# Performance work log

Hardware: AMD Instinct MI355X
Metric: run time of the kernel (lower is better)

The kernel has to match this reference:

```python
import jax, jax.numpy as jnp
import numpy as np

B, T, D = 2, 2048, 2048
H, HKV, DH = 16, 4, 128  # n_heads, n_kv_heads, d_head
EPS = 1e-6


def _rms_norm(t):
    # normalize over last dim, no learned weight (matches F.rms_norm default)
    return t * jax.lax.rsqrt(jnp.mean(t * t, axis=-1, keepdims=True) + EPS)


def _ortho_rope(t, cos, sin):
    # t: (b, h, t, d); unfold(-1,2,2) -> even/odd pairs
    x0 = t[..., 0::2]  # (b,h,t,d/2)
    x1 = t[..., 1::2]
    y0 = x0 * cos - x1 * sin
    y1 = x1 * cos + x0 * sin
    # NOTE: concatenated halves (NOT re-interleaved), faithful to source
    return jnp.concatenate((y0, y1), axis=-1)


def setup_inputs() -> dict:
    key = jax.random.key(0)
    ks = jax.random.split(key, 10)
    return {
        "x": jax.random.normal(ks[0], (B, T, D), jnp.float32),
        "pos_ids": jnp.broadcast_to(jnp.arange(T, dtype=jnp.int64), (B, T)),
        "cos": jax.random.normal(ks[1], (T, DH // 2), jnp.float32),
        "sin": jax.random.normal(ks[2], (T, DH // 2), jnp.float32),
        "v1": jax.random.normal(ks[3], (B, HKV, T, DH), jnp.float32),
        "Wq": jax.random.normal(ks[4], (H * DH, D), jnp.float32) * (D ** -0.5),
        "Wk": jax.random.normal(ks[5], (HKV * DH, D), jnp.float32) * (D ** -0.5),
        "Wv": jax.random.normal(ks[6], (HKV * DH, D), jnp.float32) * (D ** -0.5),
        "Wo": jax.random.normal(ks[7], (D, D), jnp.float32) * (D ** -0.5),
        "gate_w": jax.random.normal(ks[8], (H, H), jnp.float32) * 0.1,
        "v_lamb": jnp.float32(0.5),
    }


def reference(x, pos_ids, cos, sin, v1, Wq, Wk, Wv, Wo, gate_w, v_lamb):
    b, t, _ = x.shape
    # fused QKV projections (Linear, no bias: x @ W.T), split to heads
    q = (x @ Wq.T).reshape(b, t, H, DH).transpose(0, 2, 1, 3)    # (b,H,t,d)
    k = (x @ Wk.T).reshape(b, t, HKV, DH).transpose(0, 2, 1, 3)  # (b,Hkv,t,d)
    v = (x @ Wv.T).reshape(b, t, HKV, DH).transpose(0, 2, 1, 3)
    # value residual: lerp(v, v1, lamb) = v + lamb*(v1 - v)
    v = v + v_lamb * (v1 - v)
    # QK RMSNorm then ortho RoPE
    q = _ortho_rope(_rms_norm(q), cos, sin)
    k = _ortho_rope(_rms_norm(k), cos, sin)
    # kv_cache.upsert modeled as prefill: k,v unchanged, causal block mask
    g = H // HKV  # GQA group size
    k = jnp.repeat(k, g, axis=1)  # (b,H,t,d)
    vfull = jnp.repeat(v, g, axis=1)
    scale = DH ** -0.5
    scores = jnp.einsum('bhqd,bhkd->bhqk', q, k) * scale
    causal = jnp.tril(jnp.ones((t, t), dtype=bool))
    scores = jnp.where(causal, scores, jnp.finfo(scores.dtype).min)
    attn = jax.nn.softmax(scores, axis=-1)
    y = jnp.einsum('bhqk,bhkd->bhqd', attn, vfull)  # (b,H,t,d)
    # per-head sigmoid gate from first n_heads channels of x
    gates = jax.nn.sigmoid(x[..., :H] @ gate_w.T)   # (b,t,H)
    y = y * gates.transpose(0, 2, 1)[..., None]     # (b,H,t,1)
    y = y.transpose(0, 2, 1, 3).reshape(b, t, H * DH)
    out = y @ Wo.T
    return (out, v1)
```

## Files before the change

### kernel.cpp

```cpp
#include <hip/hip_runtime.h>

typedef __bf16 bf16;
typedef __attribute__((ext_vector_type(8))) __bf16 bf16x8;
typedef __attribute__((ext_vector_type(4))) __bf16 bf16x4;
typedef __attribute__((ext_vector_type(4))) float f32x4;
typedef __attribute__((ext_vector_type(4))) short short4v;
typedef __attribute__((ext_vector_type(4))) unsigned int u32x4;

#define BB 2
#define TT 2048
#define DD 2048
#define HH 16
#define HKV 4
#define DHD 128
#define NQKV 3072

__device__ __forceinline__ void gl_lds16(const bf16* g, bf16* l) {
    __builtin_amdgcn_global_load_lds(
        (const __attribute__((address_space(1))) void*)g,
        (__attribute__((address_space(3))) void*)l, 16, 0, 0);
}

__global__ void cvt_bf16(const float* __restrict__ src, bf16* __restrict__ dst, int n8) {
    int i = blockIdx.x * 256 + threadIdx.x;
    if (i >= n8) return;
    float4 a = ((const float4*)src)[i * 2];
    float4 b = ((const float4*)src)[i * 2 + 1];
    bf16x8 v;
    v[0] = (bf16)a.x; v[1] = (bf16)a.y; v[2] = (bf16)a.z; v[3] = (bf16)a.w;
    v[4] = (bf16)b.x; v[5] = (bf16)b.y; v[6] = (bf16)b.z; v[7] = (bf16)b.w;
    *(bf16x8*)(dst + (size_t)i * 8) = v;
}

template <int MODE>
__global__ void gemm_bt(const bf16* __restrict__ A, const bf16* __restrict__ Bw,
                        int M, int N, int K,
                        float* __restrict__ Cout,
                        bf16* __restrict__ qb, bf16* __restrict__ kb,
                        bf16* __restrict__ vtb,
                        const float* __restrict__ v1,
                        const float* __restrict__ cosb,
                        const float* __restrict__ sinb,
                        const float* __restrict__ lamp) {
    constexpr int SMEM_ELE = (MODE == 1) ? 17920 : 16384;
    __shared__ bf16 smem[SMEM_ELE];
    bf16* As = smem;
    bf16* Bs = smem + 8192;
    const int tid = threadIdx.x;
    const int w = tid >> 6, lane = tid & 63;
    const int l15 = lane & 15, quad = lane >> 4;
    const int m0 = blockIdx.y * 128, n0 = blockIdx.x * 128;
    const int wm = (w & 1) * 64, wn = (w >> 1) * 64;

    f32x4 acc[4][4] = {};
    const int lrow = lane >> 2;
    const int lcol = (lane & 3) * 8;

    for (int k0 = 0; k0 < K; k0 += 64) {
#pragma unroll
        for (int i = 0; i < 4; i++) {
            int c = w * 4 + i;
            int kc2 = c >> 3, rc = c & 7;
            int row = rc * 16 + lrow;
            int kk = k0 + kc2 * 32 + lcol;
            gl_lds16(A + (size_t)(m0 + row) * K + kk, As + c * 512);
            gl_lds16(Bw + (size_t)(n0 + row) * K + kk, Bs + c * 512);
        }
        __syncthreads();
#pragma unroll
        for (int kc2 = 0; kc2 < 2; kc2++) {
            bf16x8 af[4], bfr[4];
#pragma unroll
            for (int mi = 0; mi < 4; mi++)
                af[mi] = *(const bf16x8*)(As + kc2 * 4096 + ((wm >> 4) + mi) * 512 + l15 * 32 + quad * 8);
#pragma unroll
            for (int ni = 0; ni < 4; ni++)
                bfr[ni] = *(const bf16x8*)(Bs + kc2 * 4096 + ((wn >> 4) + ni) * 512 + l15 * 32 + quad * 8);
#pragma unroll
            for (int mi = 0; mi < 4; mi++)
#pragma unroll
                for (int ni = 0; ni < 4; ni++)
                    acc[mi][ni] = __builtin_amdgcn_mfma_f32_16x16x32_bf16(af[mi], bfr[ni], acc[mi][ni], 0, 0, 0);
        }
        __syncthreads();
    }

    if constexpr (MODE == 0) {
#pragma unroll
        for (int mi = 0; mi < 4; mi++)
#pragma unroll
            for (int ni = 0; ni < 4; ni++)
#pragma unroll
                for (int r = 0; r < 4; r++) {
                    int m = m0 + wm + mi * 16 + quad * 4 + r;
                    int n = n0 + wn + ni * 16 + l15;
                    Cout[(size_t)m * N + n] = acc[mi][ni][r];
                }
    } else {
        const int hid = n0 >> 7;
        const int b = m0 >> 11;
        const int t0 = m0 & (TT - 1);
        bf16* ep = smem;

        if (hid < 20) {
            float* ssum = (float*)(smem + 17408);
            float ssq[4][4];
#pragma unroll
            for (int mi = 0; mi < 4; mi++)
#pragma unroll
                for (int r = 0; r < 4; r++) {
                    float s = 0.f;
#pragma unroll
                    for (int ni = 0; ni < 4; ni++) {
                        float v = acc[mi][ni][r];
                        s += v * v;
                    }
                    s += __shfl_xor(s, 1);
                    s += __shfl_xor(s, 2);
                    s += __shfl_xor(s, 4);
                    s += __shfl_xor(s, 8);
                    ssq[mi][r] = s;
                }
            if (l15 == 0) {
#pragma unroll
                for (int mi = 0; mi < 4; mi++)
#pragma unroll
                    for (int r = 0; r < 4; r++)
                        ssum[(wn >> 6) * 128 + wm + mi * 16 + quad * 4 + r] = ssq[mi][r];
            }
            __syncthreads();
            const float QSCALE = 0.08838834764831845f * 1.4426950408889634f;
            float rn[4][4];
#pragma unroll
            for (int mi = 0; mi < 4; mi++)
#pragma unroll
                for (int r = 0; r < 4; r++) {
                    int row = wm + mi * 16 + quad * 4 + r;
                    float ss = ssum[row] + ssum[128 + row];
                    float rv = rsqrtf(ss * (1.f / 128.f) + 1e-6f);
                    if (hid < HH) rv *= QSCALE;
                    rn[mi][r] = rv;
                }
#pragma unroll
            for (int mi = 0; mi < 4; mi++)
#pragma unroll
                for (int ni = 0; ni < 4; ni++)
#pragma unroll
                    for (int r = 0; r < 4; r++) {
                        float sv = acc[mi][ni][r] * rn[mi][r];
                        float pv = __shfl_xor(sv, 1);
                        int nl = wn + ni * 16 + l15;
                        int j = nl >> 1;
                        int tl = wm + mi * 16 + quad * 4 + r;
                        float c = cosb[(size_t)(t0 + tl) * 64 + j];
                        float s = sinb[(size_t)(t0 + tl) * 64 + j];
                        float o = (nl & 1) ? (sv * c + pv * s) : (sv * c - pv * s);
                        int oc = (nl & 1) ? (64 + j) : j;
                        ep[tl * 136 + oc] = (bf16)o;
                    }
            __syncthreads();
            bf16* dst = (hid < HH)
                ? (qb + ((size_t)(b * HH + hid) * TT + t0) * DHD)
                : (kb + ((size_t)(b * HKV + (hid - HH)) * TT + t0) * DHD);
            int tl = tid >> 1, half = tid & 1;
#pragma unroll
            for (int c8 = 0; c8 < 8; c8++)
                *(bf16x8*)(dst + (size_t)tl * DHD + half * 64 + c8 * 8) =
                    *(const bf16x8*)(ep + tl * 136 + half * 64 + c8 * 8);
        } else {
            float lam = lamp[0];
            int vh = hid - 20;
            const float* v1b = v1 + ((size_t)(b * HKV + vh) * TT) * DHD;
#pragma unroll
            for (int mi = 0; mi < 4; mi++)
#pragma unroll
                for (int ni = 0; ni < 4; ni++)
#pragma unroll
                    for (int r = 0; r < 4; r++) {
                        int d = wn + ni * 16 + l15;
                        int tl = wm + mi * 16 + quad * 4 + r;
                        float val = acc[mi][ni][r];
                        float vm = val + lam * (v1b[(size_t)(t0 + tl) * DHD + d] - val);
                        ep[d * 136 + tl] = (bf16)vm;
                    }
            __syncthreads();
            bf16* dstv = vtb + ((size_t)(b * HKV + vh) * DHD) * TT + t0;
            int dd = tid >> 1, half = tid & 1;
#pragma unroll
            for (int c8 = 0; c8 < 8; c8++)
                *(bf16x8*)(dstv + (size_t)dd * TT + half * 64 + c8 * 8) =
                    *(const bf16x8*)(ep + dd * 136 + half * 64 + c8 * 8);
        }
    }
}

__global__ void gatesk(const float* __restrict__ x, const float* __restrict__ gw,
                       float* __restrict__ gates) {
    __shared__ float gws[256];
    gws[threadIdx.x] = gw[threadIdx.x];
    __syncthreads();
    int idx = blockIdx.x * 256 + threadIdx.x;
    int h = idx & 15, token = idx >> 4;
    const float* xr = x + (size_t)token * DD;
    float z = 0.f;
#pragma unroll
    for (int j = 0; j < 16; j++) z += xr[j] * gws[h * 16 + j];
    gates[idx] = 1.f / (1.f + __expf(-z));
}

__global__ __launch_bounds__(512, 2) void fattn(const bf16* __restrict__ qbuf,
                                                const bf16* __restrict__ kbuf,
                                                const bf16* __restrict__ vt,
                                                const float* __restrict__ gates,
                                                bf16* __restrict__ yb) {
    __shared__ bf16 Ks[2][4 * 2048];
    __shared__ bf16 VTs[2][8192];

    const int bid = blockIdx.x;
    const int bh = bid & 31;
    const int g = bid >> 5;
    const int h = bh & 15, b = bh >> 4;
    const int hk = h >> 2;
    const int tid = threadIdx.x, w = tid >> 6, lane = tid & 63;
    const int wq = w & 3, grp = w >> 2;
    const int l15 = lane & 15, quad = lane >> 4;

    const bf16* qbase = qbuf + ((size_t)(b * HH + h) * TT) * DHD;
    const bf16* kbase = kbuf + ((size_t)(b * HKV + hk) * TT) * DHD;
    const bf16* vtbase = vt + ((size_t)(b * HKV + hk) * DHD) * TT;

    const int Tq0 = grp ? (15 - g) : g;
    const int Tq1 = grp ? (16 + g) : (31 - g);
    const int ktmax_blk = 31 - g;

    bf16x8 qf0[4], qf1[4];
#pragma unroll
    for (int kc = 0; kc < 4; kc++) {
        qf0[kc] = *(const bf16x8*)(qbase + (size_t)(Tq0 * 64 + wq * 16 + l15) * DHD + kc * 32 + quad * 8);
        qf1[kc] = *(const bf16x8*)(qbase + (size_t)(Tq1 * 64 + wq * 16 + l15) * DHD + kc * 32 + quad * 8);
    }

    bool dm[4][4];
#pragma unroll
    for (int ni = 0; ni < 4; ni++)
#pragma unroll
        for (int r = 0; r < 4; r++)
            dm[ni][r] = ((ni >> 1) * 32 + quad * 8 + (ni & 1) * 4 + r) > (wq * 16 + l15);

    const int srow = lane >> 2;
    const int gst = (((lane >> 5) & 1) << 1) | ((lane >> 3) & 1);
    const int scg = ((lane & 3) ^ gst) * 8;
    const int vrow = lane >> 3;
    const int vcg = ((lane & 7) ^ ((lane >> 3) & 7)) * 8;

    auto stage = [&](int kt, int buf) {
        if (grp == 0) {
#pragma unroll
            for (int i = 0; i < 4; i++)
                gl_lds16(kbase + (size_t)(kt * 64 + wq * 16 + srow) * DHD + i * 32 + scg,
                         &Ks[buf][i * 2048 + wq * 512]);
        } else {
#pragma unroll
            for (int i = 0; i < 4; i++)
                gl_lds16(vtbase + (size_t)(wq * 32 + i * 8 + vrow) * TT + kt * 64 + vcg,
                         &VTs[buf][wq * 2048 + i * 512]);
        }
    };

    stage(0, 0);

    const int gk = (((l15 >> 2) & 1) << 1) | ((l15 >> 1) & 1);

    f32x4 O0[8] = {}, O1[8] = {};
    float m0 = -INFINITY, l0 = 0.f, m1 = -INFINITY, l1 = 0.f;

    union PW { bf16x4 h[2]; bf16x8 v; };

    for (int kt = 0; kt <= ktmax_blk; kt++) {
        int cur = kt & 1;
        __syncthreads();
        if (kt < ktmax_blk) stage(kt + 1, cur ^ 1);

        if (kt > Tq1) continue;
        const bool a0 = (kt <= Tq0);

        f32x4 s0[4], s1[4];
        __builtin_amdgcn_s_setprio(1);
#pragma unroll
        for (int ni = 0; ni < 4; ni++) {
            int rr = (ni >> 1) * 32 + (l15 >> 2) * 8 + (ni & 1) * 4 + (l15 & 3);
            bf16x8 kfl[4];
#pragma unroll
            for (int kc = 0; kc < 4; kc++)
                kfl[kc] = *(const bf16x8*)(&Ks[cur][kc * 2048 + rr * 32 + ((quad ^ gk) * 8)]);
            f32x4 z1 = {};
#pragma unroll
            for (int kc = 0; kc < 4; kc++)
                z1 = __builtin_amdgcn_mfma_f32_16x16x32_bf16(kfl[kc], qf1[kc], z1, 0, 0, 0);
            s1[ni] = z1;
            if (a0) {
                f32x4 z0 = {};
#pragma unroll
                for (int kc = 0; kc < 4; kc++)
                    z0 = __builtin_amdgcn_mfma_f32_16x16x32_bf16(kfl[kc], qf0[kc], z0, 0, 0, 0);
                s0[ni] = z0;
            }
        }
        __builtin_amdgcn_s_setprio(0);

        PW pw0[2], pw1[2];
        {
            if (kt == Tq1) {
#pragma unroll
                for (int ni = 0; ni < 4; ni++)
#pragma unroll
                    for (int r = 0; r < 4; r++)
                        if (dm[ni][r]) s1[ni][r] = -INFINITY;
            }
            float mx = s1[0][0];
#pragma unroll
            for (int ni = 0; ni < 4; ni++)
#pragma unroll
                for (int r = 0; r < 4; r++) mx = fmaxf(mx, s1[ni][r]);
            mx = fmaxf(mx, __shfl_xor(mx, 16));
            mx = fmaxf(mx, __shfl_xor(mx, 32));
            float mold = m1;
            bool noresc = __all(mx <= mold + 8.f);
            float mnew = noresc ? mold : fmaxf(mold, mx);
            float rs = 0.f;
#pragma unroll
            for (int ni = 0; ni < 4; ni++) {
                bf16x4 hv;
#pragma unroll
                for (int r = 0; r < 4; r++) {
                    float pe = __builtin_amdgcn_exp2f(s1[ni][r] - mnew);
                    hv[r] = (bf16)pe;
                    rs += pe;
                }
                pw1[ni >> 1].h[ni & 1] = hv;
            }
            rs += __shfl_xor(rs, 16);
            rs += __shfl_xor(rs, 32);
            if (!noresc) {
                float al = __builtin_amdgcn_exp2f(mold - mnew);
                l1 *= al;
#pragma unroll
                for (int dn = 0; dn < 8; dn++)
#pragma unroll
                    for (int r = 0; r < 4; r++) O1[dn][r] *= al;
                m1 = mnew;
            }
            l1 += rs;
        }
        if (a0) {
            if (kt == Tq0) {
#pragma unroll
                for (int ni = 0; ni < 4; ni++)
#pragma unroll
                    for (int r = 0; r < 4; r++)
                        if (dm[ni][r]) s0[ni][r] = -INFINITY;
            }
            float mx = s0[0][0];
#pragma unroll
            for (int ni = 0; ni < 4; ni++)
#pragma unroll
                for (int r = 0; r < 4; r++) mx = fmaxf(mx, s0[ni][r]);
            mx = fmaxf(mx, __shfl_xor(mx, 16));
            mx = fmaxf(mx, __shfl_xor(mx, 32));
            float mold = m0;
            bool noresc = __all(mx <= mold + 8.f);
            float mnew = noresc ? mold : fmaxf(mold, mx);
            float rs = 0.f;
#pragma unroll
            for (int ni = 0; ni < 4; ni++) {
                bf16x4 hv;
#pragma unroll
                for (int r = 0; r < 4; r++) {
                    float pe = __builtin_amdgcn_exp2f(s0[ni][r] - mnew);
                    hv[r] = (bf16)pe;
                    rs += pe;
                }
                pw0[ni >> 1].h[ni & 1] = hv;
            }
            rs += __shfl_xor(rs, 16);
            rs += __shfl_xor(rs, 32);
            if (!noresc) {
                float al = __builtin_amdgcn_exp2f(mold - mnew);
                l0 *= al;
#pragma unroll
                for (int dn = 0; dn < 8; dn++)
#pragma unroll
                    for (int r = 0; r < 4; r++) O0[dn][r] *= al;
                m0 = mnew;
            }
            l0 += rs;
        }

        __builtin_amdgcn_s_setprio(1);
#pragma unroll
        for (int ni2 = 0; ni2 < 2; ni2++) {
            bf16x8 vfl[8];
#pragma unroll
            for (int dn = 0; dn < 8; dn++)
                vfl[dn] = *(const bf16x8*)(&VTs[cur][(dn * 16 + l15) * 64 +
                                                    (((ni2 * 4 + quad) ^ (l15 & 7)) * 8)]);
#pragma unroll
            for (int dn = 0; dn < 8; dn++)
                O1[dn] = __builtin_amdgcn_mfma_f32_16x16x32_bf16(vfl[dn], pw1[ni2].v, O1[dn], 0, 0, 0);
            if (a0) {
#pragma unroll
                for (int dn = 0; dn < 8; dn++)
                    O0[dn] = __builtin_amdgcn_mfma_f32_16x16x32_bf16(vfl[dn], pw0[ni2].v, O0[dn], 0, 0, 0);
            }
        }
        __builtin_amdgcn_s_setprio(0);
    }

    auto epi = [&](const f32x4* Oc, float lsum, int qt) {
        int qg = qt * 64 + wq * 16 + l15;
        float gi = gates[((size_t)b * TT + qg) * HH + h] / lsum;
#pragma unroll
        for (int dn = 0; dn < 8; dn++) {
            bf16x4 o;
#pragma unroll
            for (int r = 0; r < 4; r++) o[r] = (bf16)(Oc[dn][r] * gi);
            *(bf16x4*)(yb + ((size_t)(b * TT + qg) * HH + h) * DHD + dn * 16 + quad * 4) = o;
        }
    };
    epi(O0, l0, Tq0);
    epi(O1, l1, Tq1);
}

extern "C" void kernel_launch(void* const* d_in, const int* in_sizes, int n_in,
                              void* d_out, int out_size, void* d_ws, size_t ws_size,
                              hipStream_t stream) {
    const float* x    = (const float*)d_in[0];
    const float* cosb = (const float*)d_in[2];
    const float* sinb = (const float*)d_in[3];
    const float* v1   = (const float*)d_in[4];
    const float* Wq   = (const float*)d_in[5];
    const float* Wk   = (const float*)d_in[6];
    const float* Wv   = (const float*)d_in[7];
    const float* Wo   = (const float*)d_in[8];
    const float* gw   = (const float*)d_in[9];
    const float* lam  = (const float*)d_in[10];
    float* out = (float*)d_out;

    char* ws = (char*)d_ws;
    bf16* xb     = (bf16*)(ws);
    bf16* wqkvb  = (bf16*)(ws + 16777216);
    bf16* wob    = (bf16*)(ws + 29360128);
    bf16* qb     = (bf16*)(ws + 79691776);
    bf16* kb     = (bf16*)(ws + 96468992);
    bf16* vtb    = (bf16*)(ws + 100663296);
    float* gts   = (float*)(ws + 104857600);
    bf16* yb     = xb;

    cvt_bf16<<<4096, 256, 0, stream>>>(x, xb, 1048576);
    cvt_bf16<<<2048, 256, 0, stream>>>(Wq, wqkvb, 524288);
    cvt_bf16<<<512, 256, 0, stream>>>(Wk, wqkvb + 4194304, 131072);
    cvt_bf16<<<512, 256, 0, stream>>>(Wv, wqkvb + 5242880, 131072);
    cvt_bf16<<<2048, 256, 0, stream>>>(Wo, wob, 524288);

    gemm_bt<1><<<dim3(24, 32), 256, 0, stream>>>(xb, wqkvb, 4096, NQKV, 2048,
                                                 nullptr, qb, kb, vtb, v1,
                                                 cosb, sinb, lam);
    gatesk<<<256, 256, 0, stream>>>(x, gw, gts);
    fattn<<<256, 512, 0, stream>>>(qb, kb, vtb, gts, yb);
    gemm_bt<0><<<dim3(16, 32), 256, 0, stream>>>(yb, wob, 4096, 2048, 2048,
                                                 out, nullptr, nullptr, nullptr,
                                                 nullptr, nullptr, nullptr, nullptr);
    (void)hipMemcpyAsync(out + 8388608, v1, (size_t)2097152 * sizeof(float),
                         hipMemcpyDeviceToDevice, stream);
}
```

Baseline: 312.9 us.

## Double-buffer GEMM with async LDS prefetch, swizzled layout, and 128x256 tiles

Rewrites the bf16 GEMM main loop into a software-pipelined, double-buffered scheme. Global-to-LDS loads for the next half-K stage are issued while MFMAs run on the current one, using partial vmcnt waits and raised wave priority around the MFMA block. It also XOR-swizzles the LDS layout to reduce bank conflicts and widens each block to a 128x256 tile with 512 threads, so each QKV block now handles two heads in its fused epilogue. The cost is much more LDS per block (96KB), which may limit occupancy, and fewer blocks in the grid, which may leave some CUs underused.

After: 320.4 us. 2.4% more time.

```diff
diff --git a/kernel.cpp b/kernel.cpp
--- a/kernel.cpp
+++ b/kernel.cpp
@@ -5,7 +5,6 @@
 typedef __attribute__((ext_vector_type(4))) __bf16 bf16x4;
 typedef __attribute__((ext_vector_type(4))) float f32x4;
 typedef __attribute__((ext_vector_type(4))) short short4v;
-typedef __attribute__((ext_vector_type(4))) unsigned int u32x4;
 
 #define BB 2
 #define TT 2048
@@ -33,57 +32,78 @@
 }
 
 template <int MODE>
-__global__ void gemm_bt(const bf16* __restrict__ A, const bf16* __restrict__ Bw,
-                        int M, int N, int K,
-                        float* __restrict__ Cout,
-                        bf16* __restrict__ qb, bf16* __restrict__ kb,
-                        bf16* __restrict__ vtb,
-                        const float* __restrict__ v1,
-                        const float* __restrict__ cosb,
-                        const float* __restrict__ sinb,
-                        const float* __restrict__ lamp) {
-    constexpr int SMEM_ELE = (MODE == 1) ? 17920 : 16384;
-    __shared__ bf16 smem[SMEM_ELE];
+__global__ __launch_bounds__(512, 2)
+void gemm_bt(const bf16* __restrict__ A, const bf16* __restrict__ Bw,
+             int M, int N, int K,
+             float* __restrict__ Cout,
+             bf16* __restrict__ qb, bf16* __restrict__ kb,
+             bf16* __restrict__ vtb,
+             const float* __restrict__ v1,
+             const float* __restrict__ cosb,
+             const float* __restrict__ sinb,
+             const float* __restrict__ lamp) {
+    __shared__ bf16 smem[49152];
     bf16* As = smem;
-    bf16* Bs = smem + 8192;
+    bf16* Bs = smem + 16384;
     const int tid = threadIdx.x;
     const int w = tid >> 6, lane = tid & 63;
     const int l15 = lane & 15, quad = lane >> 4;
-    const int m0 = blockIdx.y * 128, n0 = blockIdx.x * 128;
-    const int wm = (w & 1) * 64, wn = (w >> 1) * 64;
+    const int wr = w >> 2, wc = w & 3;
+    const int m0 = blockIdx.y * 128, n0 = blockIdx.x * 256;
+
+    const int sr = lane >> 2;
+    const int sc = ((lane & 3) ^ ((lane >> 3) & 3)) * 8;
+    const int tmax = (K >> 6) - 1;
 
     f32x4 acc[4][4] = {};
-    const int lrow = lane >> 2;
-    const int lcol = (lane & 3) * 8;
-
-    for (int k0 = 0; k0 < K; k0 += 64) {
-#pragma unroll
-        for (int i = 0; i < 4; i++) {
-            int c = w * 4 + i;
-            int kc2 = c >> 3, rc = c & 7;
-            int row = rc * 16 + lrow;
-            int kk = k0 + kc2 * 32 + lcol;
-            gl_lds16(A + (size_t)(m0 + row) * K + kk, As + c * 512);
-            gl_lds16(Bw + (size_t)(n0 + row) * K + kk, Bs + c * 512);
-        }
-        __syncthreads();
-#pragma unroll
-        for (int kc2 = 0; kc2 < 2; kc2++) {
-            bf16x8 af[4], bfr[4];
-#pragma unroll
-            for (int mi = 0; mi < 4; mi++)
-                af[mi] = *(const bf16x8*)(As + kc2 * 4096 + ((wm >> 4) + mi) * 512 + l15 * 32 + quad * 8);
+
+    auto stage = [&](int t, int kh) {
+        int tc = t > tmax ? tmax : t;
+        int buf = t & 1;
+        size_t kk = (size_t)(tc << 6) + (kh << 5) + sc;
+        gl_lds16(A + (size_t)(m0 + w * 16 + sr) * K + kk,
+                 As + buf * 8192 + kh * 4096 + w * 512);
+        gl_lds16(Bw + (size_t)(n0 + w * 16 + sr) * K + kk,
+                 Bs + buf * 16384 + kh * 8192 + w * 512);
+        gl_lds16(Bw + (size_t)(n0 + 128 + w * 16 + sr) * K + kk,
+                 Bs + buf * 16384 + kh * 8192 + 4096 + w * 512);
+    };
+
+    const int xs = (quad ^ ((l15 >> 1) & 3)) * 8;
+
+    auto phase = [&](int buf, int kh, int st, int skh) {
+        asm volatile("s_waitcnt vmcnt(6)" ::: "memory");
+        __builtin_amdgcn_s_barrier();
+        asm volatile("" ::: "memory");
+        bf16x8 af[4], bfr[4];
+        const bf16* Ab = As + buf * 8192 + kh * 4096;
+        const bf16* Bb = Bs + buf * 16384 + kh * 8192;
+#pragma unroll
+        for (int mi = 0; mi < 4; mi++)
+            af[mi] = *(const bf16x8*)(Ab + (wr * 64 + mi * 16 + l15) * 32 + xs);
+#pragma unroll
+        for (int ni = 0; ni < 4; ni++)
+            bfr[ni] = *(const bf16x8*)(Bb + (wc * 64 + ni * 16 + l15) * 32 + xs);
+        stage(st, skh);
+        __builtin_amdgcn_s_setprio(1);
+#pragma unroll
+        for (int mi = 0; mi < 4; mi++)
 #pragma unroll
             for (int ni = 0; ni < 4; ni++)
-                bfr[ni] = *(const bf16x8*)(Bs + kc2 * 4096 + ((wn >> 4) + ni) * 512 + l15 * 32 + quad * 8);
-#pragma unroll
-            for (int mi = 0; mi < 4; mi++)
-#pragma unroll
-                for (int ni = 0; ni < 4; ni++)
-                    acc[mi][ni] = __builtin_amdgcn_mfma_f32_16x16x32_bf16(af[mi], bfr[ni], acc[mi][ni], 0, 0, 0);
-        }
-        __syncthreads();
+                acc[mi][ni] = __builtin_amdgcn_mfma_f32_16x16x32_bf16(af[mi], bfr[ni], acc[mi][ni], 0, 0, 0);
+        __builtin_amdgcn_s_setprio(0);
+    };
+
+    stage(0, 0); stage(0, 1); stage(1, 0);
+    const int nit = K >> 7;
+    for (int i = 0; i < nit; i++) {
+        int t2 = 2 * i;
+        phase(0, 0, t2 + 1, 1);
+        phase(0, 1, t2 + 2, 0);
+        phase(1, 0, t2 + 2, 1);
+        phase(1, 1, t2 + 3, 0);
     }
+    __syncthreads();
 
     if constexpr (MODE == 0) {
 #pragma unroll
@@ -92,18 +112,18 @@
             for (int ni = 0; ni < 4; ni++)
 #pragma unroll
                 for (int r = 0; r < 4; r++) {
-                    int m = m0 + wm + mi * 16 + quad * 4 + r;
-                    int n = n0 + wn + ni * 16 + l15;
+                    int m = m0 + wr * 64 + mi * 16 + quad * 4 + r;
+                    int n = n0 + wc * 64 + ni * 16 + l15;
                     Cout[(size_t)m * N + n] = acc[mi][ni][r];
                 }
     } else {
-        const int hid = n0 >> 7;
+        const int hp = n0 >> 7;
         const int b = m0 >> 11;
         const int t0 = m0 & (TT - 1);
         bf16* ep = smem;
 
-        if (hid < 20) {
-            float* ssum = (float*)(smem + 17408);
+        if (hp < 20) {
+            float* ssum = (float*)(smem + 34816);
             float ssq[4][4];
 #pragma unroll
             for (int mi = 0; mi < 4; mi++)
@@ -126,7 +146,7 @@
                 for (int mi = 0; mi < 4; mi++)
 #pragma unroll
                     for (int r = 0; r < 4; r++)
-                        ssum[(wn >> 6) * 128 + wm + mi * 16 + quad * 4 + r] = ssq[mi][r];
+                        ssum[wc * 128 + wr * 64 + mi * 16 + quad * 4 + r] = ssq[mi][r];
             }
             __syncthreads();
             const float QSCALE = 0.08838834764831845f * 1.4426950408889634f;
@@ -135,10 +155,10 @@
             for (int mi = 0; mi < 4; mi++)
 #pragma unroll
                 for (int r = 0; r < 4; r++) {
-                    int row = wm + mi * 16 + quad * 4 + r;
-                    float ss = ssum[row] + ssum[128 + row];
+                    int row = wr * 64 + mi * 16 + quad * 4 + r;
+                    float ss = ssum[(wc & ~1) * 128 + row] + ssum[((wc & ~1) + 1) * 128 + row];
                     float rv = rsqrtf(ss * (1.f / 128.f) + 1e-6f);
-                    if (hid < HH) rv *= QSCALE;
+                    if (hp < HH) rv *= QSCALE;
                     rn[mi][r] = rv;
                 }
 #pragma unroll
@@ -149,47 +169,54 @@
                     for (int r = 0; r < 4; r++) {
                         float sv = acc[mi][ni][r] * rn[mi][r];
                         float pv = __shfl_xor(sv, 1);
-                        int nl = wn + ni * 16 + l15;
+                        int nl = (wc & 1) * 64 + ni * 16 + l15;
                         int j = nl >> 1;
-                        int tl = wm + mi * 16 + quad * 4 + r;
+                        int tl = wr * 64 + mi * 16 + quad * 4 + r;
                         float c = cosb[(size_t)(t0 + tl) * 64 + j];
                         float s = sinb[(size_t)(t0 + tl) * 64 + j];
                         float o = (nl & 1) ? (sv * c + pv * s) : (sv * c - pv * s);
                         int oc = (nl & 1) ? (64 + j) : j;
-                        ep[tl * 136 + oc] = (bf16)o;
+                        ep[(wc >> 1) * 17408 + tl * 136 + oc] = (bf16)o;
                     }
             __syncthreads();
-            bf16* dst = (hid < HH)
-                ? (qb + ((size_t)(b * HH + hid) * TT + t0) * DHD)
-                : (kb + ((size_t)(b * HKV + (hid - HH)) * TT + t0) * DHD);
-            int tl = tid >> 1, half = tid & 1;
-#pragma unroll
-            for (int c8 = 0; c8 < 8; c8++)
-                *(bf16x8*)(dst + (size_t)tl * DHD + half * 64 + c8 * 8) =
-                    *(const bf16x8*)(ep + tl * 136 + half * 64 + c8 * 8);
+            int tl = tid >> 2, sg = tid & 3;
+#pragma unroll
+            for (int hd = 0; hd < 2; hd++) {
+                int hg = hp + hd;
+                bf16* dst = (hp < HH)
+                    ? (qb + ((size_t)(b * HH + hg) * TT + t0) * DHD)
+                    : (kb + ((size_t)(b * HKV + (hg - HH)) * TT + t0) * DHD);
+#pragma unroll
+                for (int c8 = 0; c8 < 4; c8++)
+                    *(bf16x8*)(dst + (size_t)tl * DHD + sg * 8 + c8 * 32) =
+                        *(const bf16x8*)(ep + hd * 17408 + tl * 136 + sg * 8 + c8 * 32);
+            }
         } else {
             float lam = lamp[0];
-            int vh = hid - 20;
-            const float* v1b = v1 + ((size_t)(b * HKV + vh) * TT) * DHD;
 #pragma unroll
             for (int mi = 0; mi < 4; mi++)
 #pragma unroll
                 for (int ni = 0; ni < 4; ni++)
 #pragma unroll
                     for (int r = 0; r < 4; r++) {
-                        int d = wn + ni * 16 + l15;
-                        int tl = wm + mi * 16 + quad * 4 + r;
+                        int d = (wc & 1) * 64 + ni * 16 + l15;
+                        int tl = wr * 64 + mi * 16 + quad * 4 + r;
+                        int vh = hp + (wc >> 1) - 20;
                         float val = acc[mi][ni][r];
-                        float vm = val + lam * (v1b[(size_t)(t0 + tl) * DHD + d] - val);
-                        ep[d * 136 + tl] = (bf16)vm;
+                        float vm = val + lam * (v1[((size_t)(b * HKV + vh) * TT + t0 + tl) * DHD + d] - val);
+                        ep[(wc >> 1) * 17408 + d * 136 + tl] = (bf16)vm;
                     }
             __syncthreads();
-            bf16* dstv = vtb + ((size_t)(b * HKV + vh) * DHD) * TT + t0;
-            int dd = tid >> 1, half = tid & 1;
-#pragma unroll
-            for (int c8 = 0; c8 < 8; c8++)
-                *(bf16x8*)(dstv + (size_t)dd * TT + half * 64 + c8 * 8) =
-                    *(const bf16x8*)(ep + dd * 136 + half * 64 + c8 * 8);
+            int dd = tid >> 2, sg = tid & 3;
+#pragma unroll
+            for (int hd = 0; hd < 2; hd++) {
+                int vh = hp + hd - 20;
+                bf16* dstv = vtb + ((size_t)(b * HKV + vh) * DHD) * TT + t0;
+#pragma unroll
+                for (int c8 = 0; c8 < 4; c8++)
+                    *(bf16x8*)(dstv + (size_t)dd * TT + sg * 8 + c8 * 32) =
+                        *(const bf16x8*)(ep + hd * 17408 + dd * 136 + sg * 8 + c8 * 32);
+            }
         }
     }
 }
@@ -462,14 +489,14 @@
     cvt_bf16<<<512, 256, 0, stream>>>(Wv, wqkvb + 5242880, 131072);
     cvt_bf16<<<2048, 256, 0, stream>>>(Wo, wob, 524288);
 
-    gemm_bt<1><<<dim3(24, 32), 256, 0, stream>>>(xb, wqkvb, 4096, NQKV, 2048,
+    gemm_bt<1><<<dim3(12, 32), 512, 0, stream>>>(xb, wqkvb, 4096, NQKV, 2048,
                                                  nullptr, qb, kb, vtb, v1,
                                                  cosb, sinb, lam);
     gatesk<<<256, 256, 0, stream>>>(x, gw, gts);
     fattn<<<256, 512, 0, stream>>>(qb, kb, vtb, gts, yb);
-    gemm_bt<0><<<dim3(16, 32), 256, 0, stream>>>(yb, wob, 4096, 2048, 2048,
-                                                 out, nullptr, nullptr, nullptr,
-                                                 nullptr, nullptr, nullptr, nullptr);
+    gemm_bt<0><<<dim3(8, 32), 512, 0, stream>>>(yb, wob, 4096, 2048, 2048,
+                                                out, nullptr, nullptr, nullptr,
+                                                nullptr, nullptr, nullptr, nullptr);
     (void)hipMemcpyAsync(out + 8388608, v1, (size_t)2097152 * sizeof(float),
                          hipMemcpyDeviceToDevice, stream);
 }
```
